# Performance work log

Hardware: AMD Instinct MI355X
Metric: run time of the kernel (lower is better)

Reference implementation:

```python
import jax, jax.numpy as jnp
import numpy as np

BINS = 256
MIN_V = -0.25
MAX_V = 1.25
XSIGMA = 1.0 / float(np.sqrt(2.0 * np.pi))
DELTA = (MAX_V - MIN_V) / BINS
SIGMA = DELTA * XSIGMA
# constant prefactor applied once to the joint kernel: delta / (sqrt(2*pi)*sigma)
COEF = float(DELTA / (np.sqrt(2.0 * np.pi) * SIGMA))

B, N = 8, 32768


def setup_inputs() -> dict:
    key = jax.random.key(0)
    k1, k2, k3 = jax.random.split(key, 3)
    x1 = jax.random.uniform(k1, (B, N), dtype=jnp.float32)
    x2 = jax.random.uniform(k2, (B, N), dtype=jnp.float32)
    mask = jax.random.uniform(k3, (B, N), dtype=jnp.float32)
    return {"x1": x1, "x2": x2, "mask": mask}


def reference(x1, x2, mask):
    # bin centers: (bins,)
    centers = MIN_V + DELTA * (jnp.arange(BINS, dtype=x1.dtype) + 0.5)
    inv_s = 1.0 / SIGMA
    # Separable factorization of exp(-0.5*((x1-ci)^2+(x2-cj)^2)/sigma^2):
    # g1: (b, bins, N), g2: (b, bins, N) with mask folded into g2.
    d1 = (x1[:, None, :] - centers[None, :, None]) * inv_s
    d2 = (x2[:, None, :] - centers[None, :, None]) * inv_s
    g1 = jnp.exp(-0.5 * d1 * d1)
    g2 = jnp.exp(-0.5 * d2 * d2) * mask[:, None, :]
    # contract over N via batched matmul -> (b, bins, bins)
    hist = jnp.einsum("bin,bjn->bij", g1, g2)
    return COEF * hist
```

## Files before the change

kernel.cpp:

```cpp
#include <hip/hip_runtime.h>


#define BINS   256
#define NPTS   32768
#define BATCH  8
#define TROWS  8
#define NTILE  (BINS / TROWS)

static constexpr float kInvDelta = 256.0f / 1.5f;
static constexpr float kUAdd     = 0.25f * (256.0f / 1.5f) - 0.5f;
static constexpr float kPi       = 3.14159265358979323846f;

__global__ __launch_bounds__(1024) void gh_gather(
    const float* __restrict__ x1, const float* __restrict__ x2,
    const float* __restrict__ mask, float* __restrict__ out)
{
    __shared__ float tile[TROWS * BINS];
    const int tid = threadIdx.x;
    const int r0  = blockIdx.x * TROWS;
    const int b   = blockIdx.y;

    for (int i = tid; i < TROWS * BINS; i += 1024) tile[i] = 0.0f;
    __syncthreads();

    const float4* X1 = (const float4*)(x1   + b * NPTS);
    const float4* X2 = (const float4*)(x2   + b * NPTS);
    const float4* M  = (const float4*)(mask + b * NPTS);

#pragma unroll 2
    for (int it = 0; it < NPTS / 4096; ++it) {
        const int n4 = it * 1024 + tid;
        const float4 a4 = X1[n4];
        const float4 b4 = X2[n4];
        const float4 m4 = M[n4];

        const float pv1[4] = {a4.x, a4.y, a4.z, a4.w};
        const float pv2[4] = {b4.x, b4.y, b4.z, b4.w};
        const float pm[4]  = {m4.x, m4.y, m4.z, m4.w};

#pragma unroll
        for (int k = 0; k < 4; ++k) {
            const float u1 = fmaf(pv1[k], kInvDelta, kUAdd);
            const float u2 = fmaf(pv2[k], kInvDelta, kUAdd);
            const float fi = rintf(u1);
            const float fj = rintf(u2);
            const int   i0 = (int)fi;
            int         j0 = (int)fj;
            j0 = min(254, max(1, j0));
            const float t1 = u1 - fi;
            const float t2 = u2 - (float)j0;

            float w1[3], w2[3];
#pragma unroll
            for (int a = 0; a < 3; ++a) {
                const float d1 = t1 - (float)(a - 1);
                const float d2 = t2 - (float)(a - 1);
                w1[a] = __expf(-kPi * d1 * d1);
                w2[a] = __expf(-kPi * d2 * d2) * pm[k];
            }

            const int rbase = i0 - 1 - r0;
            const int cbase = j0 - 1;
#pragma unroll
            for (int a = 0; a < 3; ++a) {
                const int r = rbase + a;
                if ((unsigned)r < TROWS) {
                    const float wa  = w1[a];
                    const int   off = r * BINS + cbase;
                    atomicAdd(&tile[off + 0], wa * w2[0]);
                    atomicAdd(&tile[off + 1], wa * w2[1]);
                    atomicAdd(&tile[off + 2], wa * w2[2]);
                }
            }
        }
    }
    __syncthreads();

    float4*       o4 = (float4*)(out + ((size_t)b * BINS + r0) * BINS);
    const float4* t4 = (const float4*)tile;
    for (int i = tid; i < TROWS * BINS / 4; i += 1024) o4[i] = t4[i];
}

extern "C" void kernel_launch(void* const* d_in, const int* in_sizes, int n_in,
                              void* d_out, int out_size, void* d_ws, size_t ws_size,
                              hipStream_t stream) {
    const float* x1   = (const float*)d_in[0];
    const float* x2   = (const float*)d_in[1];
    const float* mask = (const float*)d_in[2];
    float*       out  = (float*)d_out;

    gh_gather<<<dim3(NTILE, BATCH), 1024, 0, stream>>>(x1, x2, mask, out);
}
```

Before: 80.30 us.

## Split points across chunks with larger row tiles and add reduction kernel

Enlarges each block's output row tile from 8 to 32 rows and splits the point set into 4 chunks via a third grid dimension. Each block writes a partial histogram tile to workspace, and a second kernel sums the 4 partials. This cuts the redundant reading and bin-filtering of every point by every row tile. In exchange it adds workspace traffic, a second launch, larger shared memory per block, and more LDS atomic contention per tile.

```diff
diff --git a/kernel.cpp b/kernel.cpp
--- a/kernel.cpp
+++ b/kernel.cpp
@@ -4,31 +4,35 @@
 #define BINS   256
 #define NPTS   32768
 #define BATCH  8
-#define TROWS  8
+#define TROWS  32
 #define NTILE  (BINS / TROWS)
+#define CHUNK  4
+#define PPC    (NPTS / CHUNK)
+#define TILEF  (TROWS * BINS)
 
 static constexpr float kInvDelta = 256.0f / 1.5f;
 static constexpr float kUAdd     = 0.25f * (256.0f / 1.5f) - 0.5f;
 static constexpr float kPi       = 3.14159265358979323846f;
 
-__global__ __launch_bounds__(1024) void gh_gather(
+__global__ __launch_bounds__(1024) void gh_part(
     const float* __restrict__ x1, const float* __restrict__ x2,
-    const float* __restrict__ mask, float* __restrict__ out)
+    const float* __restrict__ mask, float* __restrict__ ws)
 {
-    __shared__ float tile[TROWS * BINS];
+    __shared__ float tile[TILEF];
     const int tid = threadIdx.x;
     const int r0  = blockIdx.x * TROWS;
     const int b   = blockIdx.y;
+    const int z   = blockIdx.z;
 
-    for (int i = tid; i < TROWS * BINS; i += 1024) tile[i] = 0.0f;
+    for (int i = tid; i < TILEF; i += 1024) tile[i] = 0.0f;
     __syncthreads();
 
-    const float4* X1 = (const float4*)(x1   + b * NPTS);
-    const float4* X2 = (const float4*)(x2   + b * NPTS);
-    const float4* M  = (const float4*)(mask + b * NPTS);
+    const float4* X1 = (const float4*)(x1   + b * NPTS + z * PPC);
+    const float4* X2 = (const float4*)(x2   + b * NPTS + z * PPC);
+    const float4* M  = (const float4*)(mask + b * NPTS + z * PPC);
 
-#pragma unroll 2
-    for (int it = 0; it < NPTS / 4096; ++it) {
+#pragma unroll
+    for (int it = 0; it < PPC / 4096; ++it) {
         const int n4 = it * 1024 + tid;
         const float4 a4 = X1[n4];
         const float4 b4 = X2[n4];
@@ -76,9 +80,35 @@
     }
     __syncthreads();
 
-    float4*       o4 = (float4*)(out + ((size_t)b * BINS + r0) * BINS);
+    float4*       o4 = (float4*)(ws + (size_t)(((b * NTILE + blockIdx.x) * CHUNK + z)) * TILEF);
     const float4* t4 = (const float4*)tile;
-    for (int i = tid; i < TROWS * BINS / 4; i += 1024) o4[i] = t4[i];
+    for (int i = tid; i < TILEF / 4; i += 1024) o4[i] = t4[i];
+}
+
+__global__ __launch_bounds__(1024) void gh_reduce(
+    const float* __restrict__ ws, float* __restrict__ out)
+{
+    const int g    = blockIdx.x * 1024 + threadIdx.x;
+    const int flat = g * 4;
+    const int b    = flat >> 16;
+    const int rem  = flat & 65535;
+    const int r    = rem >> 8;
+    const int c    = rem & 255;
+    const int t    = r >> 5;
+    const int rr   = r & 31;
+
+    const float4* W = (const float4*)(ws + (size_t)((b * NTILE + t) * CHUNK) * TILEF
+                                         + rr * BINS + c);
+    const float4 p0 = W[0];
+    const float4 p1 = W[2048];
+    const float4 p2 = W[4096];
+    const float4 p3 = W[6144];
+    float4 s;
+    s.x = (p0.x + p1.x) + (p2.x + p3.x);
+    s.y = (p0.y + p1.y) + (p2.y + p3.y);
+    s.z = (p0.z + p1.z) + (p2.z + p3.z);
+    s.w = (p0.w + p1.w) + (p2.w + p3.w);
+    ((float4*)out)[g] = s;
 }
 
 extern "C" void kernel_launch(void* const* d_in, const int* in_sizes, int n_in,
@@ -88,6 +118,8 @@
     const float* x2   = (const float*)d_in[1];
     const float* mask = (const float*)d_in[2];
     float*       out  = (float*)d_out;
+    float*       ws   = (float*)d_ws;
 
-    gh_gather<<<dim3(NTILE, BATCH), 1024, 0, stream>>>(x1, x2, mask, out);
+    gh_part<<<dim3(NTILE, BATCH, CHUNK), 1024, 0, stream>>>(x1, x2, mask, ws);
+    gh_reduce<<<dim3(BATCH * BINS * BINS / 4096), 1024, 0, stream>>>(ws, out);
 }
```

Result: slower. 84.02 us (+4.6%).

## Accumulate histogram in packed fixed-point 64-bit LDS atomics

Applied to the files above, without the earlier changes.

Replaces the per-bin float LDS atomics with unsigned 32-bit fixed-point values (scale 1024), packed two per 64-bit word. Each row update now needs two 64-bit atomic adds over an even-aligned 4-column window, instead of three float atomics over 3 columns. The aim is fewer LDS atomic operations per point. In exchange it computes one extra exponential per point, adds float-to-int conversions, and quantizes each contribution to 1/1024, which introduces rounding error. It also relies on the low 32-bit lane never overflowing into the high lane.

```diff
diff --git a/kernel.cpp b/kernel.cpp
--- a/kernel.cpp
+++ b/kernel.cpp
@@ -6,21 +6,24 @@
 #define BATCH  8
 #define TROWS  8
 #define NTILE  (BINS / TROWS)
+#define TILE64 (TROWS * BINS / 2)
 
 static constexpr float kInvDelta = 256.0f / 1.5f;
 static constexpr float kUAdd     = 0.25f * (256.0f / 1.5f) - 0.5f;
 static constexpr float kPi       = 3.14159265358979323846f;
+static constexpr float kFix      = 1024.0f;
+static constexpr float kInvFix   = 1.0f / 1024.0f;
 
 __global__ __launch_bounds__(1024) void gh_gather(
     const float* __restrict__ x1, const float* __restrict__ x2,
     const float* __restrict__ mask, float* __restrict__ out)
 {
-    __shared__ float tile[TROWS * BINS];
+    __shared__ unsigned long long tile[TILE64];
     const int tid = threadIdx.x;
     const int r0  = blockIdx.x * TROWS;
     const int b   = blockIdx.y;
 
-    for (int i = tid; i < TROWS * BINS; i += 1024) tile[i] = 0.0f;
+    tile[tid] = 0ULL;
     __syncthreads();
 
     const float4* X1 = (const float4*)(x1   + b * NPTS);
@@ -43,42 +46,57 @@
             const float u1 = fmaf(pv1[k], kInvDelta, kUAdd);
             const float u2 = fmaf(pv2[k], kInvDelta, kUAdd);
             const float fi = rintf(u1);
-            const float fj = rintf(u2);
             const int   i0 = (int)fi;
-            int         j0 = (int)fj;
-            j0 = min(254, max(1, j0));
             const float t1 = u1 - fi;
-            const float t2 = u2 - (float)j0;
 
-            float w1[3], w2[3];
+            int e = (((int)rintf(u2)) - 1) & ~1;
+            e = min(252, max(0, e));
+            const float t2 = u2 - (float)e;
+
+            float w1a[3];
 #pragma unroll
             for (int a = 0; a < 3; ++a) {
-                const float d1 = t1 - (float)(a - 1);
-                const float d2 = t2 - (float)(a - 1);
-                w1[a] = __expf(-kPi * d1 * d1);
-                w2[a] = __expf(-kPi * d2 * d2) * pm[k];
+                const float d = t1 - (float)(a - 1);
+                w1a[a] = __expf(-kPi * d * d);
+            }
+            float W2[4];
+#pragma unroll
+            for (int c = 0; c < 4; ++c) {
+                const float d = t2 - (float)c;
+                W2[c] = __expf(-kPi * d * d) * (pm[k] * kFix);
             }
 
             const int rbase = i0 - 1 - r0;
-            const int cbase = j0 - 1;
+            const int pcol  = e >> 1;
 #pragma unroll
             for (int a = 0; a < 3; ++a) {
                 const int r = rbase + a;
                 if ((unsigned)r < TROWS) {
-                    const float wa  = w1[a];
-                    const int   off = r * BINS + cbase;
-                    atomicAdd(&tile[off + 0], wa * w2[0]);
-                    atomicAdd(&tile[off + 1], wa * w2[1]);
-                    atomicAdd(&tile[off + 2], wa * w2[2]);
+                    const float wa = w1a[a];
+                    union { unsigned long long u; uint2 v; } p0, p1;
+                    p0.v.x = (unsigned)fmaf(wa, W2[0], 0.5f);
+                    p0.v.y = (unsigned)fmaf(wa, W2[1], 0.5f);
+                    p1.v.x = (unsigned)fmaf(wa, W2[2], 0.5f);
+                    p1.v.y = (unsigned)fmaf(wa, W2[3], 0.5f);
+                    const int idx = r * (BINS / 2) + pcol;
+                    atomicAdd(&tile[idx + 0], p0.u);
+                    atomicAdd(&tile[idx + 1], p1.u);
                 }
             }
         }
     }
     __syncthreads();
 
-    float4*       o4 = (float4*)(out + ((size_t)b * BINS + r0) * BINS);
-    const float4* t4 = (const float4*)tile;
-    for (int i = tid; i < TROWS * BINS / 4; i += 1024) o4[i] = t4[i];
+    {
+        const unsigned long long v = tile[tid];
+        const int r = tid >> 7;
+        const int p = tid & 127;
+        float2 f;
+        f.x = (float)(unsigned)(v & 0xffffffffULL) * kInvFix;
+        f.y = (float)(unsigned)(v >> 32)           * kInvFix;
+        float2* o2 = (float2*)(out + ((size_t)b * BINS + r0 + r) * BINS);
+        o2[p] = f;
+    }
 }
 
 extern "C" void kernel_launch(void* const* d_in, const int* in_sizes, int n_in,
```

Result: faster. 78.26 us (-2.5%).

## Split points across blocks with packed 16-bit fixed-point LDS atomics and a reduce pass

Applied to the files above, without the earlier changes.

Each block now owns a chunk of points and half of the histogram rows, instead of every block scanning all points for an 8-row strip. Weights are quantized to fixed point (scale 1024) and three adjacent columns are packed into one 64-bit integer atomic. The neighbour exponentials come from a recurrence using one exp and a reciprocal, which saves exp calls. A second kernel sums the 32 partial tiles per batch and converts back to float. This removes the redundant per-strip rereads and filtering of every point and cuts the atomic count. In exchange it adds quantization error, risks 16-bit lane overflow, writes a large workspace to global memory and needs an extra launch.

```diff
diff --git a/kernel.cpp b/kernel.cpp
--- a/kernel.cpp
+++ b/kernel.cpp
@@ -4,81 +4,114 @@
 #define BINS   256
 #define NPTS   32768
 #define BATCH  8
-#define TROWS  8
-#define NTILE  (BINS / TROWS)
+#define CHUNK  32
+#define PPB    (NPTS / CHUNK)
+#define HROWS  128
+#define WROW   64
+#define TILE64 (HROWS * WROW)
+#define NBLK   (BATCH * CHUNK * 2)
 
 static constexpr float kInvDelta = 256.0f / 1.5f;
 static constexpr float kUAdd     = 0.25f * (256.0f / 1.5f) - 0.5f;
 static constexpr float kPi       = 3.14159265358979323846f;
+static constexpr float kTwoPi    = 6.28318530717958647692f;
+static constexpr float kEmPi     = 0.043213918263772250f;
+static constexpr float kFix      = 1024.0f;
+static constexpr float kInvFix   = 1.0f / 1024.0f;
 
-__global__ __launch_bounds__(1024) void gh_gather(
+__global__ __launch_bounds__(1024) void gh_part(
     const float* __restrict__ x1, const float* __restrict__ x2,
-    const float* __restrict__ mask, float* __restrict__ out)
+    const float* __restrict__ mask, unsigned long long* __restrict__ ws)
 {
-    __shared__ float tile[TROWS * BINS];
+    __shared__ unsigned long long lds[TILE64];
     const int tid = threadIdx.x;
-    const int r0  = blockIdx.x * TROWS;
-    const int b   = blockIdx.y;
+    const int h   = blockIdx.x & 1;
+    const int z   = (blockIdx.x >> 1) & 31;
+    const int b   = blockIdx.x >> 6;
+    const int rb  = h * HROWS;
 
-    for (int i = tid; i < TROWS * BINS; i += 1024) tile[i] = 0.0f;
+#pragma unroll
+    for (int i = tid; i < TILE64; i += 1024) lds[i] = 0ULL;
     __syncthreads();
 
-    const float4* X1 = (const float4*)(x1   + b * NPTS);
-    const float4* X2 = (const float4*)(x2   + b * NPTS);
-    const float4* M  = (const float4*)(mask + b * NPTS);
+    const int n = b * NPTS + z * PPB + tid;
+    const float xv = x1[n];
+    const float yv = x2[n];
+    const float mv = mask[n];
 
-#pragma unroll 2
-    for (int it = 0; it < NPTS / 4096; ++it) {
-        const int n4 = it * 1024 + tid;
-        const float4 a4 = X1[n4];
-        const float4 b4 = X2[n4];
-        const float4 m4 = M[n4];
+    const float u1 = fmaf(xv, kInvDelta, kUAdd);
+    const float u2 = fmaf(yv, kInvDelta, kUAdd);
+    int i0 = (int)rintf(u1); i0 = min(254, max(1, i0));
+    int j0 = (int)rintf(u2); j0 = min(252, max(1, j0));
+    const float t1 = u1 - (float)i0;
+    const float t2 = u2 - (float)j0;
 
-        const float pv1[4] = {a4.x, a4.y, a4.z, a4.w};
-        const float pv2[4] = {b4.x, b4.y, b4.z, b4.w};
-        const float pm[4]  = {m4.x, m4.y, m4.z, m4.w};
+    const float w0  = __expf(-kPi * t1 * t1);
+    const float G1  = __expf(-kTwoPi * t1);
+    const float iG1 = __builtin_amdgcn_rcpf(G1);
+    const float w0K = w0 * kEmPi;
+    const float wr[3] = { w0K * G1, w0, w0K * iG1 };
+
+    const float vc  = __expf(-kPi * t2 * t2) * (mv * kFix);
+    const float G2  = __expf(-kTwoPi * t2);
+    const float iG2 = __builtin_amdgcn_rcpf(G2);
+    const float vcK = vc * kEmPi;
+    const float v0 = vcK * G2, v1 = vc, v2 = vcK * iG2;
+
+    const int c0   = j0 - 1;
+    const int word = c0 >> 2;
+    const int sh   = 16 * (c0 & 3);
 
 #pragma unroll
-        for (int k = 0; k < 4; ++k) {
-            const float u1 = fmaf(pv1[k], kInvDelta, kUAdd);
-            const float u2 = fmaf(pv2[k], kInvDelta, kUAdd);
-            const float fi = rintf(u1);
-            const float fj = rintf(u2);
-            const int   i0 = (int)fi;
-            int         j0 = (int)fj;
-            j0 = min(254, max(1, j0));
-            const float t1 = u1 - fi;
-            const float t2 = u2 - (float)j0;
-
-            float w1[3], w2[3];
-#pragma unroll
-            for (int a = 0; a < 3; ++a) {
-                const float d1 = t1 - (float)(a - 1);
-                const float d2 = t2 - (float)(a - 1);
-                w1[a] = __expf(-kPi * d1 * d1);
-                w2[a] = __expf(-kPi * d2 * d2) * pm[k];
-            }
-
-            const int rbase = i0 - 1 - r0;
-            const int cbase = j0 - 1;
-#pragma unroll
-            for (int a = 0; a < 3; ++a) {
-                const int r = rbase + a;
-                if ((unsigned)r < TROWS) {
-                    const float wa  = w1[a];
-                    const int   off = r * BINS + cbase;
-                    atomicAdd(&tile[off + 0], wa * w2[0]);
-                    atomicAdd(&tile[off + 1], wa * w2[1]);
-                    atomicAdd(&tile[off + 2], wa * w2[2]);
-                }
-            }
+    for (int a = 0; a < 3; ++a) {
+        const int rloc = i0 - 1 + a - rb;
+        if ((unsigned)rloc < HROWS) {
+            const float wa = wr[a];
+            const unsigned f0 = (unsigned)fmaf(wa, v0, 0.5f);
+            const unsigned f1 = (unsigned)fmaf(wa, v1, 0.5f);
+            const unsigned f2 = (unsigned)fmaf(wa, v2, 0.5f);
+            const unsigned long long q =
+                (unsigned long long)f0 | ((unsigned long long)f1 << 16)
+                                       | ((unsigned long long)f2 << 32);
+            const unsigned long long lo = q << sh;
+            const unsigned long long hi = (q >> 1) >> (63 - sh);
+            atomicAdd(&lds[rloc * WROW + word], lo);
+            if (hi) atomicAdd(&lds[rloc * WROW + word + 1], hi);
         }
     }
     __syncthreads();
 
-    float4*       o4 = (float4*)(out + ((size_t)b * BINS + r0) * BINS);
-    const float4* t4 = (const float4*)tile;
-    for (int i = tid; i < TROWS * BINS / 4; i += 1024) o4[i] = t4[i];
+    unsigned long long* W = ws + (size_t)blockIdx.x * TILE64;
+#pragma unroll
+    for (int i = tid; i < TILE64; i += 1024) W[i] = lds[i];
+}
+
+__global__ __launch_bounds__(512) void gh_reduce(
+    const unsigned long long* __restrict__ ws, float* __restrict__ out)
+{
+    const int wp  = blockIdx.x * 512 + threadIdx.x;
+    const int b   = wp >> 14;
+    const int w   = wp & 16383;
+    const int row = w >> 6;
+    const int h   = row >> 7;
+    const int wl  = (row & (HROWS - 1)) * WROW + (w & 63);
+
+    unsigned s0 = 0, s1 = 0, s2 = 0, s3 = 0;
+#pragma unroll
+    for (int z = 0; z < CHUNK; ++z) {
+        const unsigned long long v =
+            ws[(size_t)(((b * CHUNK + z) << 1) + h) * TILE64 + wl];
+        s0 += (unsigned)v & 0xFFFFu;
+        s1 += (unsigned)(v >> 16) & 0xFFFFu;
+        s2 += (unsigned)(v >> 32) & 0xFFFFu;
+        s3 += (unsigned)(v >> 48);
+    }
+    float4 o;
+    o.x = (float)s0 * kInvFix;
+    o.y = (float)s1 * kInvFix;
+    o.z = (float)s2 * kInvFix;
+    o.w = (float)s3 * kInvFix;
+    ((float4*)out)[wp] = o;
 }
 
 extern "C" void kernel_launch(void* const* d_in, const int* in_sizes, int n_in,
@@ -88,6 +121,8 @@
     const float* x2   = (const float*)d_in[1];
     const float* mask = (const float*)d_in[2];
     float*       out  = (float*)d_out;
+    unsigned long long* ws = (unsigned long long*)d_ws;
 
-    gh_gather<<<dim3(NTILE, BATCH), 1024, 0, stream>>>(x1, x2, mask, out);
+    gh_part  <<<dim3(NBLK), 1024, 0, stream>>>(x1, x2, mask, ws);
+    gh_reduce<<<dim3(BATCH * BINS * WROW / 512), 512, 0, stream>>>(ws, out);
 }
```

Result: faster. 75.92 us (-5.5%).
